# Optimization experiments

Hardware: AMD Instinct MI355X
Metric: run time of the kernel (lower is better)

Reference implementation:

```python
import jax, jax.numpy as jnp
import numpy as np

NUM_EXPERTS = 8
TOP_K = 2
N_EMBD = 1024
BLOCKING = 128
D_FFN = ((4 * N_EMBD // TOP_K) + BLOCKING - 1) // BLOCKING * BLOCKING  # 2048


def setup_inputs() -> dict:
    key = jax.random.key(0)
    k_x, k_r, k_w1, k_w2 = jax.random.split(key, 4)
    B, S = 4, 2048
    x = jax.random.normal(k_x, (B, S, N_EMBD), dtype=jnp.float32)
    # nn.Linear weight layout: [out_features, in_features]
    router_w = jax.random.normal(k_r, (NUM_EXPERTS, N_EMBD), dtype=jnp.float32) * 0.02
    # trunc_normal(std=0.02, a=-0.06, b=0.06) approximated by clipped normal
    w1 = jnp.clip(jax.random.normal(k_w1, (N_EMBD, NUM_EXPERTS * D_FFN), dtype=jnp.float32) * 0.02, -0.06, 0.06)
    w2 = jnp.clip(jax.random.normal(k_w2, (NUM_EXPERTS * D_FFN, N_EMBD), dtype=jnp.float32) * 0.02, -0.06, 0.06)
    return {"x": x, "router_w": router_w, "w1": w1, "w2": w2}


def reference(x, router_w, w1, w2):
    B, S, D = x.shape
    T = B * S
    x_flat = x.reshape(T, D)

    # Router
    router_logits = x_flat @ router_w.T                       # [T, E]
    router_probs = jax.nn.softmax(router_logits.astype(jnp.float32), axis=-1)
    expert_weights, selected_experts = jax.lax.top_k(router_probs, TOP_K)  # [T, K]
    expert_weights = expert_weights / expert_weights.sum(axis=-1, keepdims=True)
    expert_weights = expert_weights.astype(x.dtype)

    # Combine weights c[t, e] = sum_k weight[t, k] * [sel[t, k] == e]
    combine = jnp.zeros((T, NUM_EXPERTS), dtype=x.dtype)
    combine = combine.at[jnp.arange(T)[:, None], selected_experts].add(expert_weights)

    # Expert FFNs (math equivalent of block-sparse sdd/gelu/dsd + scatter-combine)
    w1r = w1.reshape(D, NUM_EXPERTS, D_FFN)
    w2r = w2.reshape(NUM_EXPERTS, D_FFN, D)
    out_flat = jnp.zeros((T, D), dtype=x.dtype)
    for e in range(NUM_EXPERTS):
        h = jax.nn.gelu(x_flat @ w1r[:, e, :], approximate=False)  # [T, d_ffn]
        out_flat = out_flat + combine[:, e:e + 1] * (h @ w2r[e])
    output = out_flat.reshape(B, S, D)

    # Aux losses
    router_z_loss = jnp.mean(jax.nn.logsumexp(router_logits, axis=-1) ** 2)
    p_i = router_probs.mean(axis=0)                           # [E]
    f_i = jnp.zeros((NUM_EXPERTS,), dtype=x.dtype).at[selected_experts.reshape(-1)].add(
        jnp.float32(1.0) / (T * TOP_K))
    load_balance_loss = NUM_EXPERTS * jnp.dot(f_i, p_i.astype(x.dtype))

    return output, router_z_loss, load_balance_loss, f_i
```

## Files before the change

kernel.cpp:

```cpp
#include <hip/hip_runtime.h>
#include <hip/hip_bf16.h>
#include <math.h>

#define T_TOK   8192
#define D_MODEL 1024
#define DFFN    2048
#define N_EXP   8
#define NASSIGN (T_TOK*2)

#define BM 128
#define BN 128
#define BK 64
#define TILE_MAX 144

#define WS_ZSUM     0
#define WS_PSUM     4
#define WS_COUNTS   64
#define WS_CURSOR   96
#define WS_OFFS     128
#define WS_NTILES   160
#define WS_TMAP     256
#define WS_SEL      4096
#define WS_WGT      69632
#define WS_AIDX     135168
#define WS_AW       200704
#define WS_XB       266240
#define WS_W1T      (WS_XB + 16777216)
#define WS_W2T      (WS_W1T + 33554432)
#define WS_H        (WS_W2T + 33554432)

typedef __attribute__((ext_vector_type(8))) short bf16x8;
typedef __attribute__((ext_vector_type(4))) float f32x4;
typedef __attribute__((ext_vector_type(4))) unsigned int u32x4;

static __device__ __forceinline__ unsigned short f2bf(float f) {
    unsigned int u = __builtin_bit_cast(unsigned int, f);
    u += 0x7fffu + ((u >> 16) & 1u);
    return (unsigned short)(u >> 16);
}

static __device__ __forceinline__ void gll16(const unsigned short* g, unsigned short* l) {
    __builtin_amdgcn_global_load_lds(
        (const __attribute__((address_space(1))) unsigned int*)g,
        (__attribute__((address_space(3))) unsigned int*)l, 16, 0, 0);
}

static __device__ __forceinline__ int frag_off(int row, int kc) {
    return (row * 8 + (kc ^ (row & 7))) * 8;
}

__global__ __launch_bounds__(256) void transpose_cvt_kernel(
    const float* __restrict__ in, unsigned short* __restrict__ out, int K, int N)
{
    int e = blockIdx.z;
    const float* inp = in + (size_t)e * K * N;
    unsigned short* outp = out + (size_t)e * K * N;
    __shared__ unsigned short tile[64][68];
    int k0 = blockIdx.y * 64, n0 = blockIdx.x * 64;
    int tid = threadIdx.x;
    int r = tid >> 4, c4 = (tid & 15) * 4;
    #pragma unroll
    for (int p = 0; p < 4; ++p) {
        int k = r + p * 16;
        float4 v = *(const float4*)(inp + (size_t)(k0 + k) * N + n0 + c4);
        tile[k][c4+0] = f2bf(v.x);
        tile[k][c4+1] = f2bf(v.y);
        tile[k][c4+2] = f2bf(v.z);
        tile[k][c4+3] = f2bf(v.w);
    }
    __syncthreads();
    int n = tid >> 2, kc = (tid & 3) * 16;
    unsigned short t[16];
    #pragma unroll
    for (int j = 0; j < 16; ++j) t[j] = tile[kc + j][n];
    unsigned short* o = outp + (size_t)(n0 + n) * K + k0 + kc;
    *(u32x4*)o       = *(u32x4*)t;
    *(u32x4*)(o + 8) = *(u32x4*)(t + 8);
}

__global__ __launch_bounds__(256) void router_kernel(
    const float* __restrict__ x, const float* __restrict__ rw,
    float* zsum, float* psum, int* counts, int* sel, float* wgt,
    unsigned short* __restrict__ xb)
{
    __shared__ float xs[32*129];
    __shared__ float rs[8*129];
    __shared__ float lg[32*9];
    __shared__ float blk_p[8];
    __shared__ int   blk_c[8];
    __shared__ float blk_z;
    int tid = threadIdx.x;
    if (tid < 8) { blk_p[tid] = 0.f; blk_c[tid] = 0; }
    if (tid == 8) blk_z = 0.f;
    int tb = blockIdx.x * 32;
    int tt = tid >> 3, e = tid & 7;
    float acc = 0.f;
    for (int c = 0; c < 8; ++c) {
        int c0 = c * 128;
        #pragma unroll
        for (int p = 0; p < 16; ++p) {
            int flat = p * 256 + tid;
            int r = flat >> 7, col = flat & 127;
            xs[r*129 + col] = x[(size_t)(tb + r)*D_MODEL + c0 + col];
        }
        #pragma unroll
        for (int p = 0; p < 4; ++p) {
            int flat = p * 256 + tid;
            int er = flat >> 7, col = flat & 127;
            rs[er*129 + col] = rw[(size_t)er*D_MODEL + c0 + col];
        }
        __syncthreads();
        {
            int rr = tid >> 3, cc = (tid & 7) * 16;
            unsigned short tmp[16];
            #pragma unroll
            for (int j = 0; j < 16; ++j) tmp[j] = f2bf(xs[rr*129 + cc + j]);
            unsigned short* o = xb + (size_t)(tb + rr)*D_MODEL + c0 + cc;
            *(u32x4*)o       = *(u32x4*)tmp;
            *(u32x4*)(o + 8) = *(u32x4*)(tmp + 8);
        }
        #pragma unroll 8
        for (int i = 0; i < 128; ++i)
            acc += xs[tt*129 + i] * rs[e*129 + i];
        __syncthreads();
    }
    lg[tt*9 + e] = acc;
    __syncthreads();
    if (tid < 32) {
        int t = tb + tid;
        float l[8], p[8];
        float mx = -1e30f;
        #pragma unroll
        for (int j = 0; j < 8; ++j) { l[j] = lg[tid*9 + j]; mx = fmaxf(mx, l[j]); }
        float se = 0.f;
        #pragma unroll
        for (int j = 0; j < 8; ++j) { p[j] = expf(l[j] - mx); se += p[j]; }
        float inv = 1.f / se;
        #pragma unroll
        for (int j = 0; j < 8; ++j) p[j] *= inv;
        float lse = mx + logf(se);
        atomicAdd(&blk_z, lse*lse);
        #pragma unroll
        for (int j = 0; j < 8; ++j) atomicAdd(&blk_p[j], p[j]);
        int i0 = 0; float b0 = p[0];
        #pragma unroll
        for (int j = 1; j < 8; ++j) if (p[j] > b0) { b0 = p[j]; i0 = j; }
        int i1 = -1; float b1 = -1.f;
        #pragma unroll
        for (int j = 0; j < 8; ++j) if (j != i0 && p[j] > b1) { b1 = p[j]; i1 = j; }
        float s = b0 + b1;
        sel[t*2+0] = i0; sel[t*2+1] = i1;
        wgt[t*2+0] = b0 / s; wgt[t*2+1] = b1 / s;
        atomicAdd(&blk_c[i0], 1); atomicAdd(&blk_c[i1], 1);
    }
    __syncthreads();
    if (tid < 8) {
        atomicAdd(&counts[tid], blk_c[tid]);
        unsafeAtomicAdd(&psum[tid], blk_p[tid]);
    }
    if (tid == 8) unsafeAtomicAdd(zsum, blk_z);
}

__global__ void finalize_kernel(const int* counts, const float* psum, const float* zsum,
                                int* offs, int* ntiles, int* tmap, float* out_tail)
{
    if (threadIdx.x != 0) return;
    int off = 0, nt = 0;
    float lb = 0.f;
    for (int e = 0; e < N_EXP; ++e) {
        int c = counts[e];
        offs[e] = off;
        for (int m0 = 0; m0 < c; m0 += BM) {
            tmap[nt*4+0] = e;
            tmap[nt*4+1] = off + m0;
            tmap[nt*4+2] = min(BM, c - m0);
            tmap[nt*4+3] = 0;
            nt++;
        }
        float fi = (float)c / (float)NASSIGN;
        out_tail[2 + e] = fi;
        lb += fi * (psum[e] / (float)T_TOK);
        off += c;
    }
    *ntiles = nt;
    out_tail[0] = zsum[0] / (float)T_TOK;
    out_tail[1] = (float)N_EXP * lb;
}

__global__ __launch_bounds__(256) void scatter_kernel(
    const int* __restrict__ sel, const float* __restrict__ wgt,
    const int* __restrict__ offs, int* cursor, int* aidx, float* aw)
{
    int t = blockIdx.x * 256 + threadIdx.x;
    if (t >= T_TOK) return;
    #pragma unroll
    for (int k = 0; k < 2; ++k) {
        int e = sel[t*2 + k];
        int pos = atomicAdd(&cursor[e], 1);
        int r = offs[e] + pos;
        aidx[r] = t;
        aw[r] = wgt[t*2 + k];
    }
}

__global__ __launch_bounds__(256) void gemm1_kernel(
    const unsigned short* __restrict__ xb, const unsigned short* __restrict__ w1t,
    const int* __restrict__ aidx, const int* __restrict__ tmap,
    const int* __restrict__ ntiles, unsigned short* __restrict__ H)
{
    int tile = blockIdx.y;
    if (tile >= *ntiles) return;
    int e     = tmap[tile*4+0];
    int gr    = tmap[tile*4+1];
    int valid = tmap[tile*4+2];
    int n0 = blockIdx.x * BN;
    __shared__ unsigned short As[BM*BK];
    __shared__ unsigned short Bs[BN*BK];
    int tid = threadIdx.x;
    int lane = tid & 63, wave = tid >> 6;
    int wm = (wave & 1) * 64, wn = (wave >> 1) * 64;
    int q = lane >> 4, r16 = lane & 15;
    f32x4 acc[4][4];
    #pragma unroll
    for (int i = 0; i < 4; ++i)
        #pragma unroll
        for (int j = 0; j < 4; ++j) acc[i][j] = (f32x4){0.f, 0.f, 0.f, 0.f};

    const unsigned short* aga[4];
    const unsigned short* bga[4];
    unsigned short* ldsA[4];
    unsigned short* ldsB[4];
    #pragma unroll
    for (int j = 0; j < 4; ++j) {
        int c = tid + j*256;
        int m = c >> 3, kl = c & 7;
        int kg = kl ^ (m & 7);
        int tok = aidx[gr + min(m, valid - 1)];
        aga[j] = xb + (size_t)tok * D_MODEL + kg*8;
        bga[j] = w1t + ((size_t)(e * DFFN + n0 + m)) * D_MODEL + kg*8;
        ldsA[j] = As + c*8;
        ldsB[j] = Bs + c*8;
    }

    for (int kt = 0; kt < D_MODEL / BK; ++kt) {
        int ko = kt * BK;
        #pragma unroll
        for (int j = 0; j < 4; ++j) gll16(aga[j] + ko, ldsA[j]);
        #pragma unroll
        for (int j = 0; j < 4; ++j) gll16(bga[j] + ko, ldsB[j]);
        __syncthreads();
        #pragma unroll
        for (int kh = 0; kh < 2; ++kh) {
            bf16x8 af[4], bfr[4];
            #pragma unroll
            for (int im = 0; im < 4; ++im)
                af[im] = *(const bf16x8*)&As[frag_off(wm + im*16 + r16, q + 4*kh)];
            #pragma unroll
            for (int in = 0; in < 4; ++in)
                bfr[in] = *(const bf16x8*)&Bs[frag_off(wn + in*16 + r16, q + 4*kh)];
            #pragma unroll
            for (int im = 0; im < 4; ++im)
                #pragma unroll
                for (int in = 0; in < 4; ++in)
                    acc[im][in] = __builtin_amdgcn_mfma_f32_16x16x32_bf16(af[im], bfr[in], acc[im][in], 0, 0, 0);
        }
        __syncthreads();
    }
    #pragma unroll
    for (int im = 0; im < 4; ++im) {
        #pragma unroll
        for (int reg = 0; reg < 4; ++reg) {
            int m = wm + im*16 + q*4 + reg;
            if (m < valid) {
                size_t rowbase = (size_t)(gr + m) * DFFN + n0 + wn;
                #pragma unroll
                for (int in = 0; in < 4; ++in) {
                    float v = acc[im][in][reg];
                    float g = 0.5f * v * (1.0f + erff(v * 0.70710678118654752f));
                    H[rowbase + in*16 + r16] = f2bf(g);
                }
            }
        }
    }
}

__global__ __launch_bounds__(256) void gemm2_kernel(
    const unsigned short* __restrict__ H, const unsigned short* __restrict__ w2t,
    const int* __restrict__ aidx, const float* __restrict__ aw,
    const int* __restrict__ tmap, const int* __restrict__ ntiles,
    float* __restrict__ out)
{
    int tile = blockIdx.y;
    if (tile >= *ntiles) return;
    int e     = tmap[tile*4+0];
    int gr    = tmap[tile*4+1];
    int valid = tmap[tile*4+2];
    int n0 = blockIdx.x * BN;
    __shared__ unsigned short As[BM*BK];
    __shared__ unsigned short Bs[BN*BK];
    int tid = threadIdx.x;
    int lane = tid & 63, wave = tid >> 6;
    int wm = (wave & 1) * 64, wn = (wave >> 1) * 64;
    int q = lane >> 4, r16 = lane & 15;
    f32x4 acc[4][4];
    #pragma unroll
    for (int i = 0; i < 4; ++i)
        #pragma unroll
        for (int j = 0; j < 4; ++j) acc[i][j] = (f32x4){0.f, 0.f, 0.f, 0.f};

    const unsigned short* aga[4];
    const unsigned short* bga[4];
    unsigned short* ldsA[4];
    unsigned short* ldsB[4];
    #pragma unroll
    for (int j = 0; j < 4; ++j) {
        int c = tid + j*256;
        int m = c >> 3, kl = c & 7;
        int kg = kl ^ (m & 7);
        aga[j] = H + (size_t)(gr + min(m, valid - 1)) * DFFN + kg*8;
        bga[j] = w2t + (size_t)e * (DFFN * D_MODEL) + (size_t)(n0 + m) * DFFN + kg*8;
        ldsA[j] = As + c*8;
        ldsB[j] = Bs + c*8;
    }

    for (int kt = 0; kt < DFFN / BK; ++kt) {
        int ko = kt * BK;
        #pragma unroll
        for (int j = 0; j < 4; ++j) gll16(aga[j] + ko, ldsA[j]);
        #pragma unroll
        for (int j = 0; j < 4; ++j) gll16(bga[j] + ko, ldsB[j]);
        __syncthreads();
        #pragma unroll
        for (int kh = 0; kh < 2; ++kh) {
            bf16x8 af[4], bfr[4];
            #pragma unroll
            for (int im = 0; im < 4; ++im)
                af[im] = *(const bf16x8*)&As[frag_off(wm + im*16 + r16, q + 4*kh)];
            #pragma unroll
            for (int in = 0; in < 4; ++in)
                bfr[in] = *(const bf16x8*)&Bs[frag_off(wn + in*16 + r16, q + 4*kh)];
            #pragma unroll
            for (int im = 0; im < 4; ++im)
                #pragma unroll
                for (int in = 0; in < 4; ++in)
                    acc[im][in] = __builtin_amdgcn_mfma_f32_16x16x32_bf16(af[im], bfr[in], acc[im][in], 0, 0, 0);
        }
        __syncthreads();
    }
    #pragma unroll
    for (int im = 0; im < 4; ++im) {
        #pragma unroll
        for (int reg = 0; reg < 4; ++reg) {
            int m = wm + im*16 + q*4 + reg;
            if (m < valid) {
                int t = aidx[gr + m];
                float w = aw[gr + m];
                float* orow = out + (size_t)t*D_MODEL + n0 + wn;
                #pragma unroll
                for (int in = 0; in < 4; ++in)
                    unsafeAtomicAdd(&orow[in*16 + r16], w * acc[im][in][reg]);
            }
        }
    }
}

extern "C" void kernel_launch(void* const* d_in, const int* in_sizes, int n_in,
                              void* d_out, int out_size, void* d_ws, size_t ws_size,
                              hipStream_t stream)
{
    const float* x  = (const float*)d_in[0];
    const float* rw = (const float*)d_in[1];
    const float* w1 = (const float*)d_in[2];
    const float* w2 = (const float*)d_in[3];
    float* out = (float*)d_out;
    char* ws = (char*)d_ws;
    float* zsum   = (float*)(ws + WS_ZSUM);
    float* psum   = (float*)(ws + WS_PSUM);
    int*   counts = (int*)(ws + WS_COUNTS);
    int*   cursor = (int*)(ws + WS_CURSOR);
    int*   offs   = (int*)(ws + WS_OFFS);
    int*   ntiles = (int*)(ws + WS_NTILES);
    int*   tmap   = (int*)(ws + WS_TMAP);
    int*   sel    = (int*)(ws + WS_SEL);
    float* wgt    = (float*)(ws + WS_WGT);
    int*   aidx   = (int*)(ws + WS_AIDX);
    float* aw     = (float*)(ws + WS_AW);
    unsigned short* xb  = (unsigned short*)(ws + WS_XB);
    unsigned short* w1t = (unsigned short*)(ws + WS_W1T);
    unsigned short* w2t = (unsigned short*)(ws + WS_W2T);
    unsigned short* H   = (unsigned short*)(ws + WS_H);

    hipMemsetAsync(d_out, 0, (size_t)T_TOK * D_MODEL * sizeof(float), stream);
    hipMemsetAsync(ws, 0, 256, stream);

    transpose_cvt_kernel<<<dim3(16384/64, 1024/64, 1), 256, 0, stream>>>(w1, w1t, 1024, 16384);
    transpose_cvt_kernel<<<dim3(1024/64, 2048/64, 8), 256, 0, stream>>>(w2, w2t, 2048, 1024);

    router_kernel<<<T_TOK/32, 256, 0, stream>>>(x, rw, zsum, psum, counts, sel, wgt, xb);
    finalize_kernel<<<1, 64, 0, stream>>>(counts, psum, zsum, offs, ntiles, tmap,
                                          out + (size_t)T_TOK * D_MODEL);
    scatter_kernel<<<T_TOK/256, 256, 0, stream>>>(sel, wgt, offs, cursor, aidx, aw);
    gemm1_kernel<<<dim3(DFFN/BN, TILE_MAX), 256, 0, stream>>>(xb, w1t, aidx, tmap, ntiles, H);
    gemm2_kernel<<<dim3(D_MODEL/BN, TILE_MAX), 256, 0, stream>>>(H, w2t, aidx, aw, tmap, ntiles, out);
}
```

Measured before the change: 597.2 us.

## Double-buffer GEMM LDS tiles with BK=32 and XCD-aware tile remapping

Both expert GEMMs move to a two-stage LDS double buffer with BK=32, so the next K-slice is fetched by direct global-to-LDS loads while MFMAs run on the current one, using explicit vmcnt waits and raw barriers. The LDS layout switches from an XOR-swizzled layout to a k-chunk-major layout. Block indices are also remapped so that each XCD handles a contiguous run of tiles, which is meant to improve L2 reuse of expert weights. The risks are more barriers per unit of work because K-steps are smaller, possible LDS bank conflicts without the swizzle, and a remap that hard-codes TILE_MAX=144 split as 8×18.

```diff
diff --git a/kernel.cpp b/kernel.cpp
--- a/kernel.cpp
+++ b/kernel.cpp
@@ -10,7 +10,7 @@
 
 #define BM 128
 #define BN 128
-#define BK 64
+#define BK 32
 #define TILE_MAX 144
 
 #define WS_ZSUM     0
@@ -45,10 +45,6 @@
         (__attribute__((address_space(3))) unsigned int*)l, 16, 0, 0);
 }
 
-static __device__ __forceinline__ int frag_off(int row, int kc) {
-    return (row * 8 + (kc ^ (row & 7))) * 8;
-}
-
 __global__ __launch_bounds__(256) void transpose_cvt_kernel(
     const float* __restrict__ in, unsigned short* __restrict__ out, int K, int N)
 {
@@ -208,14 +204,17 @@
     const int* __restrict__ aidx, const int* __restrict__ tmap,
     const int* __restrict__ ntiles, unsigned short* __restrict__ H)
 {
-    int tile = blockIdx.y;
+    int f = blockIdx.y * 16 + blockIdx.x;
+    int xcd = f & 7, s = f >> 3;
+    int tile = xcd * 18 + (s >> 4);
+    int xblk = s & 15;
     if (tile >= *ntiles) return;
     int e     = tmap[tile*4+0];
     int gr    = tmap[tile*4+1];
     int valid = tmap[tile*4+2];
-    int n0 = blockIdx.x * BN;
-    __shared__ unsigned short As[BM*BK];
-    __shared__ unsigned short Bs[BN*BK];
+    int n0 = xblk * BN;
+    __shared__ unsigned short As[2][4*128*8];
+    __shared__ unsigned short Bs[2][4*128*8];
     int tid = threadIdx.x;
     int lane = tid & 63, wave = tid >> 6;
     int wm = (wave & 1) * 64, wn = (wave >> 1) * 64;
@@ -226,45 +225,47 @@
         #pragma unroll
         for (int j = 0; j < 4; ++j) acc[i][j] = (f32x4){0.f, 0.f, 0.f, 0.f};
 
-    const unsigned short* aga[4];
-    const unsigned short* bga[4];
-    unsigned short* ldsA[4];
-    unsigned short* ldsB[4];
-    #pragma unroll
-    for (int j = 0; j < 4; ++j) {
-        int c = tid + j*256;
-        int m = c >> 3, kl = c & 7;
-        int kg = kl ^ (m & 7);
-        int tok = aidx[gr + min(m, valid - 1)];
-        aga[j] = xb + (size_t)tok * D_MODEL + kg*8;
-        bga[j] = w1t + ((size_t)(e * DFFN + n0 + m)) * D_MODEL + kg*8;
-        ldsA[j] = As + c*8;
-        ldsB[j] = Bs + c*8;
-    }
-
-    for (int kt = 0; kt < D_MODEL / BK; ++kt) {
-        int ko = kt * BK;
-        #pragma unroll
-        for (int j = 0; j < 4; ++j) gll16(aga[j] + ko, ldsA[j]);
-        #pragma unroll
-        for (int j = 0; j < 4; ++j) gll16(bga[j] + ko, ldsB[j]);
-        __syncthreads();
-        #pragma unroll
-        for (int kh = 0; kh < 2; ++kh) {
-            bf16x8 af[4], bfr[4];
-            #pragma unroll
-            for (int im = 0; im < 4; ++im)
-                af[im] = *(const bf16x8*)&As[frag_off(wm + im*16 + r16, q + 4*kh)];
+    int row = tid & 127, half = tid >> 7;
+    int tok = aidx[gr + min(row, valid - 1)];
+    const unsigned short* gA = xb + (size_t)tok * D_MODEL + half * 8;
+    const unsigned short* gB = w1t + ((size_t)(e * DFFN + n0 + row)) * D_MODEL + half * 8;
+    unsigned short* lA0[2]; unsigned short* lA1[2];
+    unsigned short* lB0[2]; unsigned short* lB1[2];
+    #pragma unroll
+    for (int b = 0; b < 2; ++b) {
+        lA0[b] = &As[b][(half*128 + row)*8];
+        lA1[b] = &As[b][((2+half)*128 + row)*8];
+        lB0[b] = &Bs[b][(half*128 + row)*8];
+        lB1[b] = &Bs[b][((2+half)*128 + row)*8];
+    }
+
+    const int KT = D_MODEL / BK;
+    gll16(gA, lA0[0]); gll16(gA + 16, lA1[0]);
+    gll16(gB, lB0[0]); gll16(gB + 16, lB1[0]);
+    for (int kt = 0; kt < KT; ++kt) {
+        int b = kt & 1;
+        if (kt + 1 < KT) {
+            int ko = (kt + 1) * BK;
+            gll16(gA + ko, lA0[b^1]); gll16(gA + ko + 16, lA1[b^1]);
+            gll16(gB + ko, lB0[b^1]); gll16(gB + ko + 16, lB1[b^1]);
+            asm volatile("s_waitcnt vmcnt(4)" ::: "memory");
+        } else {
+            asm volatile("s_waitcnt vmcnt(0)" ::: "memory");
+        }
+        asm volatile("s_barrier" ::: "memory");
+        bf16x8 af[4], bfr[4];
+        #pragma unroll
+        for (int im = 0; im < 4; ++im)
+            af[im] = *(const bf16x8*)&As[b][(q*128 + wm + im*16 + r16)*8];
+        #pragma unroll
+        for (int in = 0; in < 4; ++in)
+            bfr[in] = *(const bf16x8*)&Bs[b][(q*128 + wn + in*16 + r16)*8];
+        #pragma unroll
+        for (int im = 0; im < 4; ++im)
             #pragma unroll
             for (int in = 0; in < 4; ++in)
-                bfr[in] = *(const bf16x8*)&Bs[frag_off(wn + in*16 + r16, q + 4*kh)];
-            #pragma unroll
-            for (int im = 0; im < 4; ++im)
-                #pragma unroll
-                for (int in = 0; in < 4; ++in)
-                    acc[im][in] = __builtin_amdgcn_mfma_f32_16x16x32_bf16(af[im], bfr[in], acc[im][in], 0, 0, 0);
-        }
-        __syncthreads();
+                acc[im][in] = __builtin_amdgcn_mfma_f32_16x16x32_bf16(af[im], bfr[in], acc[im][in], 0, 0, 0);
+        if (kt + 1 < KT) asm volatile("s_barrier" ::: "memory");
     }
     #pragma unroll
     for (int im = 0; im < 4; ++im) {
@@ -290,14 +291,17 @@
     const int* __restrict__ tmap, const int* __restrict__ ntiles,
     float* __restrict__ out)
 {
-    int tile = blockIdx.y;
+    int f = blockIdx.y * 8 + blockIdx.x;
+    int xcd = f & 7, s = f >> 3;
+    int tile = xcd * 18 + (s >> 3);
+    int xblk = s & 7;
     if (tile >= *ntiles) return;
     int e     = tmap[tile*4+0];
     int gr    = tmap[tile*4+1];
     int valid = tmap[tile*4+2];
-    int n0 = blockIdx.x * BN;
-    __shared__ unsigned short As[BM*BK];
-    __shared__ unsigned short Bs[BN*BK];
+    int n0 = xblk * BN;
+    __shared__ unsigned short As[2][4*128*8];
+    __shared__ unsigned short Bs[2][4*128*8];
     int tid = threadIdx.x;
     int lane = tid & 63, wave = tid >> 6;
     int wm = (wave & 1) * 64, wn = (wave >> 1) * 64;
@@ -308,44 +312,46 @@
         #pragma unroll
         for (int j = 0; j < 4; ++j) acc[i][j] = (f32x4){0.f, 0.f, 0.f, 0.f};
 
-    const unsigned short* aga[4];
-    const unsigned short* bga[4];
-    unsigned short* ldsA[4];
-    unsigned short* ldsB[4];
-    #pragma unroll
-    for (int j = 0; j < 4; ++j) {
-        int c = tid + j*256;
-        int m = c >> 3, kl = c & 7;
-        int kg = kl ^ (m & 7);
-        aga[j] = H + (size_t)(gr + min(m, valid - 1)) * DFFN + kg*8;
-        bga[j] = w2t + (size_t)e * (DFFN * D_MODEL) + (size_t)(n0 + m) * DFFN + kg*8;
-        ldsA[j] = As + c*8;
-        ldsB[j] = Bs + c*8;
-    }
-
-    for (int kt = 0; kt < DFFN / BK; ++kt) {
-        int ko = kt * BK;
-        #pragma unroll
-        for (int j = 0; j < 4; ++j) gll16(aga[j] + ko, ldsA[j]);
-        #pragma unroll
-        for (int j = 0; j < 4; ++j) gll16(bga[j] + ko, ldsB[j]);
-        __syncthreads();
-        #pragma unroll
-        for (int kh = 0; kh < 2; ++kh) {
-            bf16x8 af[4], bfr[4];
-            #pragma unroll
-            for (int im = 0; im < 4; ++im)
-                af[im] = *(const bf16x8*)&As[frag_off(wm + im*16 + r16, q + 4*kh)];
+    int row = tid & 127, half = tid >> 7;
+    const unsigned short* gA = H + (size_t)(gr + min(row, valid - 1)) * DFFN + half * 8;
+    const unsigned short* gB = w2t + (size_t)e * (DFFN * D_MODEL) + (size_t)(n0 + row) * DFFN + half * 8;
+    unsigned short* lA0[2]; unsigned short* lA1[2];
+    unsigned short* lB0[2]; unsigned short* lB1[2];
+    #pragma unroll
+    for (int b = 0; b < 2; ++b) {
+        lA0[b] = &As[b][(half*128 + row)*8];
+        lA1[b] = &As[b][((2+half)*128 + row)*8];
+        lB0[b] = &Bs[b][(half*128 + row)*8];
+        lB1[b] = &Bs[b][((2+half)*128 + row)*8];
+    }
+
+    const int KT = DFFN / BK;
+    gll16(gA, lA0[0]); gll16(gA + 16, lA1[0]);
+    gll16(gB, lB0[0]); gll16(gB + 16, lB1[0]);
+    for (int kt = 0; kt < KT; ++kt) {
+        int b = kt & 1;
+        if (kt + 1 < KT) {
+            int ko = (kt + 1) * BK;
+            gll16(gA + ko, lA0[b^1]); gll16(gA + ko + 16, lA1[b^1]);
+            gll16(gB + ko, lB0[b^1]); gll16(gB + ko + 16, lB1[b^1]);
+            asm volatile("s_waitcnt vmcnt(4)" ::: "memory");
+        } else {
+            asm volatile("s_waitcnt vmcnt(0)" ::: "memory");
+        }
+        asm volatile("s_barrier" ::: "memory");
+        bf16x8 af[4], bfr[4];
+        #pragma unroll
+        for (int im = 0; im < 4; ++im)
+            af[im] = *(const bf16x8*)&As[b][(q*128 + wm + im*16 + r16)*8];
+        #pragma unroll
+        for (int in = 0; in < 4; ++in)
+            bfr[in] = *(const bf16x8*)&Bs[b][(q*128 + wn + in*16 + r16)*8];
+        #pragma unroll
+        for (int im = 0; im < 4; ++im)
             #pragma unroll
             for (int in = 0; in < 4; ++in)
-                bfr[in] = *(const bf16x8*)&Bs[frag_off(wn + in*16 + r16, q + 4*kh)];
-            #pragma unroll
-            for (int im = 0; im < 4; ++im)
-                #pragma unroll
-                for (int in = 0; in < 4; ++in)
-                    acc[im][in] = __builtin_amdgcn_mfma_f32_16x16x32_bf16(af[im], bfr[in], acc[im][in], 0, 0, 0);
-        }
-        __syncthreads();
+                acc[im][in] = __builtin_amdgcn_mfma_f32_16x16x32_bf16(af[im], bfr[in], acc[im][in], 0, 0, 0);
+        if (kt + 1 < KT) asm volatile("s_barrier" ::: "memory");
     }
     #pragma unroll
     for (int im = 0; im < 4; ++im) {
@@ -400,6 +406,6 @@
     finalize_kernel<<<1, 64, 0, stream>>>(counts, psum, zsum, offs, ntiles, tmap,
                                           out + (size_t)T_TOK * D_MODEL);
     scatter_kernel<<<T_TOK/256, 256, 0, stream>>>(sel, wgt, offs, cursor, aidx, aw);
-    gemm1_kernel<<<dim3(DFFN/BN, TILE_MAX), 256, 0, stream>>>(xb, w1t, aidx, tmap, ntiles, H);
-    gemm2_kernel<<<dim3(D_MODEL/BN, TILE_MAX), 256, 0, stream>>>(H, w2t, aidx, aw, tmap, ntiles, out);
-}
+    gemm1_kernel<<<dim3(16, TILE_MAX), 256, 0, stream>>>(xb, w1t, aidx, tmap, ntiles, H);
+    gemm2_kernel<<<dim3(8, TILE_MAX), 256, 0, stream>>>(H, w2t, aidx, aw, tmap, ntiles, out);
+}
```

Measured after the change: 663.2 us. 1.11x slower.
